# Kernel optimization log

Hardware: AMD Instinct MI355X
Metric: run time of the kernel (lower is better)

Reference implementation:

```python
import jax, jax.numpy as jnp
import numpy as np

N_NODES = 50000
N_EDGES = 800000
N_FEAT = 128
HIDDEN = 256
N_CLASSES = 40
K_HOPS = 10
ALPHA = 0.1


def setup_inputs() -> dict:
    key = jax.random.key(0)
    k1, k2, k3, k4 = jax.random.split(key, 4)
    x = jax.random.normal(k1, (N_NODES, N_FEAT), dtype=jnp.float32)
    edge_index = jax.random.randint(k2, (2, N_EDGES), 0, N_NODES, dtype=jnp.int64)
    # PPR init of gamma weights: temp[k] = alpha*(1-alpha)^k, temp[K] = (1-alpha)^K
    temp_np = ALPHA * (1.0 - ALPHA) ** np.arange(K_HOPS + 1)
    temp_np[-1] = (1.0 - ALPHA) ** K_HOPS
    temp = jnp.asarray(temp_np, dtype=jnp.float32)
    W1 = jax.random.normal(k3, (N_FEAT, HIDDEN), dtype=jnp.float32) * (1.0 / np.sqrt(N_FEAT))
    b1 = jnp.zeros((HIDDEN,), dtype=jnp.float32)
    W2 = jax.random.normal(k4, (HIDDEN, N_CLASSES), dtype=jnp.float32) * (1.0 / np.sqrt(HIDDEN))
    b2 = jnp.zeros((N_CLASSES,), dtype=jnp.float32)
    return {"x": x, "edge_index": edge_index, "temp": temp,
            "W1": W1, "b1": b1, "W2": W2, "b2": b2, "K": K_HOPS}


def reference(x, edge_index, temp, W1, b1, W2, b2, K):
    N = x.shape[0]
    # gcn_norm with self-loops (fill value 1): A_hat = D^-1/2 (A + I) D^-1/2
    loops = jnp.arange(N, dtype=edge_index.dtype)
    row = jnp.concatenate([edge_index[0], loops])  # source (x_j)
    col = jnp.concatenate([edge_index[1], loops])  # target (aggregation)
    ones = jnp.ones(row.shape[0], dtype=x.dtype)
    deg = jax.ops.segment_sum(ones, col, num_segments=N)
    dinv = jnp.where(deg > 0, deg ** -0.5, jnp.zeros_like(deg))
    norm = dinv[row] * dinv[col]  # [E+N]

    # K-hop propagation with learned hop-weighted sum
    h = x
    hidden = temp[0] * x
    for k in range(K):  # small fixed hop count
        msg = norm[:, None] * h[row]                      # gather + scale
        h = jax.ops.segment_sum(msg, col, num_segments=N)  # scatter-add
        hidden = hidden + temp[k + 1] * h

    # eval mode: dropout is a no-op
    z = jax.nn.relu(hidden @ W1 + b1)
    z = z @ W2 + b2
    return jax.nn.log_softmax(z, axis=1)
```

## Files before the change

kernel.cpp:

```cpp
#include <hip/hip_runtime.h>
#include <hip/hip_bf16.h>


#define NFEAT 128
#define HID   256
#define NCLS  40
#define KHOPS 10

typedef __attribute__((ext_vector_type(8))) short short8;
typedef __attribute__((ext_vector_type(4))) float floatx4;

__device__ __forceinline__ float blo(unsigned g) { return __uint_as_float(g << 16); }
__device__ __forceinline__ float bhi(unsigned g) { return __uint_as_float(g & 0xffff0000u); }
__device__ __forceinline__ unsigned f2bf(float x) {
  unsigned u = __float_as_uint(x);
  return (u + 0x7fffu + ((u >> 16) & 1u)) >> 16;
}
__device__ __forceinline__ unsigned bpack(float a, float b) {
  return f2bf(a) | (f2bf(b) << 16);
}

__global__ void k_detect64(const unsigned int* __restrict__ raw, int* __restrict__ flag) {
  __shared__ int any;
  int t = threadIdx.x;
  if (t == 0) any = 0;
  __syncthreads();
  if (raw[2 * t + 1] != 0u) any = 1;
  __syncthreads();
  if (t == 0) flag[0] = (any == 0) ? 1 : 0;
}

__global__ void k_zero(int* __restrict__ p, int n) {
  int i = blockIdx.x * blockDim.x + threadIdx.x;
  if (i < n) p[i] = 0;
}

__global__ void k_count(const int* __restrict__ ei32, const long long* __restrict__ ei64,
                        int E, int N, int* __restrict__ cnt, int* __restrict__ rank,
                        const int* __restrict__ flag) {
  int e = blockIdx.x * blockDim.x + threadIdx.x;
  if (e >= E) return;
  int dst = flag[0] ? (int)ei64[(size_t)E + e] : ei32[(size_t)E + e];
  if ((unsigned)dst < (unsigned)N) rank[e] = atomicAdd(&cnt[dst], 1);
  else rank[e] = -1;
}

__global__ __launch_bounds__(256) void k_scan_a(
    const int* __restrict__ cnt, int* __restrict__ bsum, int n) {
  int t = threadIdx.x;
  int base = blockIdx.x * 1024 + t * 4;
  int s = 0;
  if (base + 3 < n) {
    int4 v = *(const int4*)(cnt + base);
    s = v.x + v.y + v.z + v.w;
  } else {
    #pragma unroll
    for (int j = 0; j < 4; ++j) if (base + j < n) s += cnt[base + j];
  }
  #pragma unroll
  for (int off = 1; off < 64; off <<= 1) s += __shfl_xor(s, off);
  __shared__ int ws[4];
  if ((t & 63) == 0) ws[t >> 6] = s;
  __syncthreads();
  if (t == 0) bsum[blockIdx.x] = ws[0] + ws[1] + ws[2] + ws[3];
}

__global__ void k_scan_mid(int* __restrict__ bsum, int* __restrict__ S,
                           int ntiles, int n) {
  int t = threadIdx.x;
  int lane = t & 63, wid = t >> 6;
  int v = (t < ntiles) ? bsum[t] : 0;
  int x = v;
  #pragma unroll
  for (int off = 1; off < 64; off <<= 1) {
    int u = __shfl_up(x, off);
    if (lane >= off) x += u;
  }
  __shared__ int ws[16];
  if (lane == 63) ws[wid] = x;
  __syncthreads();
  if (wid == 0) {
    int s2 = (lane < 16) ? ws[lane] : 0;
    #pragma unroll
    for (int off = 1; off < 16; off <<= 1) {
      int u = __shfl_up(s2, off);
      if (lane >= off) s2 += u;
    }
    if (lane < 16) ws[lane] = s2;
  }
  __syncthreads();
  int woff = wid ? ws[wid - 1] : 0;
  if (t < ntiles) bsum[t] = x - v + woff;
  if (t == 0) S[n] = ws[15];
}

__global__ __launch_bounds__(256) void k_scan_c(
    const int* __restrict__ cnt, const int* __restrict__ bsum,
    int* __restrict__ S, float* __restrict__ dinv, int n) {
  int t = threadIdx.x;
  int base = blockIdx.x * 1024 + t * 4;
  int v[4];
  if (base + 3 < n) {
    int4 q = *(const int4*)(cnt + base);
    v[0] = q.x; v[1] = q.y; v[2] = q.z; v[3] = q.w;
  } else {
    #pragma unroll
    for (int j = 0; j < 4; ++j) v[j] = (base + j < n) ? cnt[base + j] : 0;
  }
  int tsum = v[0] + v[1] + v[2] + v[3];
  int lane = t & 63, wv = t >> 6;
  int x = tsum;
  #pragma unroll
  for (int off = 1; off < 64; off <<= 1) {
    int u = __shfl_up(x, off);
    if (lane >= off) x += u;
  }
  __shared__ int ws[4];
  if (lane == 63) ws[wv] = x;
  __syncthreads();
  int woff = 0;
  #pragma unroll
  for (int j = 0; j < 4; ++j) if (j < wv) woff += ws[j];
  int run = x - tsum + woff + bsum[blockIdx.x];
  #pragma unroll
  for (int j = 0; j < 4; ++j) {
    int idx = base + j;
    if (idx < n) {
      S[idx] = run;
      dinv[idx] = rsqrtf((float)(v[j] + 1));
      run += v[j];
    }
  }
}

__global__ void k_fill(const int* __restrict__ ei32, const long long* __restrict__ ei64,
                       int E, int N, const int* __restrict__ S,
                       const int* __restrict__ rank, int* __restrict__ csr,
                       const int* __restrict__ flag) {
  int e = blockIdx.x * blockDim.x + threadIdx.x;
  if (e >= E) return;
  int r = rank[e];
  if (r < 0) return;
  int src, dst;
  if (flag[0]) { src = (int)ei64[e]; dst = (int)ei64[(size_t)E + e]; }
  else         { src = ei32[e];      dst = ei32[(size_t)E + e]; }
  if ((unsigned)src >= (unsigned)N) return;
  csr[S[dst] + r] = src;
}

__global__ void k_init(const float* __restrict__ x, const float* __restrict__ temp,
                       const float* __restrict__ dinv,
                       unsigned* __restrict__ h2, float* __restrict__ hidden,
                       int total64) {
  int i = blockIdx.x * blockDim.x + threadIdx.x;
  if (i >= total64) return;
  float2 xv = ((const float2*)x)[i];
  float di = dinv[i >> 6];
  h2[i] = bpack(di * xv.x, di * xv.y);
  float t0 = temp[0];
  ((float2*)hidden)[i] = make_float2(t0 * xv.x, t0 * xv.y);
}

__global__ __launch_bounds__(256) void k_prop(
    const unsigned* __restrict__ h2, unsigned* __restrict__ hnew2,
    float* __restrict__ hidden,
    const int* __restrict__ S, const int* __restrict__ csr,
    const float* __restrict__ dinv, const float* __restrict__ temp,
    int k, int N, int mode) {
  int wid = __builtin_amdgcn_readfirstlane(threadIdx.x >> 6);
  int lane = threadIdx.x & 63;
  int node = blockIdx.x * 4 + wid;
  if (node >= N) return;
  int g = lane & 15;
  int e = lane >> 4;
  int s = S[node], en = S[node + 1];
  float acc[8] = {0.f, 0.f, 0.f, 0.f, 0.f, 0.f, 0.f, 0.f};
  for (int p = s; p < en; p += 16) {
    uint4 gd[4];
    float wt[4];
    #pragma unroll
    for (int t = 0; t < 4; ++t) {
      int pj = p + t * 4 + e;
      int sidx = csr[pj < en ? pj : s];
      wt[t] = (pj < en) ? 1.f : 0.f;
      gd[t] = *(const uint4*)(h2 + (size_t)sidx * 64 + g * 4);
    }
    #pragma unroll
    for (int t = 0; t < 4; ++t) {
      const unsigned* gu = (const unsigned*)&gd[t];
      #pragma unroll
      for (int u = 0; u < 4; ++u) {
        acc[u * 2]     += wt[t] * blo(gu[u]);
        acc[u * 2 + 1] += wt[t] * bhi(gu[u]);
      }
    }
  }
  #pragma unroll
  for (int u = 0; u < 8; ++u) {
    acc[u] += __shfl_xor(acc[u], 16);
    acc[u] += __shfl_xor(acc[u], 32);
  }
  if (e == 0) {
    float di = dinv[node];
    uint4 gs = *(const uint4*)(h2 + (size_t)node * 64 + g * 4);
    const unsigned* su = (const unsigned*)&gs;
    #pragma unroll
    for (int u = 0; u < 4; ++u) {
      acc[u * 2]     += blo(su[u]);
      acc[u * 2 + 1] += bhi(su[u]);
    }
    float hn[8];
    #pragma unroll
    for (int u = 0; u < 8; ++u) hn[u] = di * acc[u];
    float tk = temp[k + 1];
    float4* hp = (float4*)(hidden + (size_t)node * NFEAT + g * 8);
    float4 h0 = hp[0], h1 = hp[1];
    h0.x += tk * hn[0];  h0.y += tk * hn[1];
    h0.z += tk * hn[2];  h0.w += tk * hn[3];
    h1.x += tk * hn[4];  h1.y += tk * hn[5];
    h1.z += tk * hn[6];  h1.w += tk * hn[7];
    uint4 pk;
    if (mode == 0) {
      pk.x = bpack(di * hn[0], di * hn[1]);
      pk.y = bpack(di * hn[2], di * hn[3]);
      pk.z = bpack(di * hn[4], di * hn[5]);
      pk.w = bpack(di * hn[6], di * hn[7]);
      *(uint4*)(hnew2 + (size_t)node * 64 + g * 4) = pk;
      hp[0] = h0;  hp[1] = h1;
    } else {
      pk.x = bpack(h0.x, h0.y);  pk.y = bpack(h0.z, h0.w);
      pk.z = bpack(h1.x, h1.y);  pk.w = bpack(h1.z, h1.w);
      *(uint4*)(hnew2 + (size_t)node * 64 + g * 4) = pk;
    }
  }
}

__global__ __launch_bounds__(256) void k_gemm1(
    const unsigned short* __restrict__ Ab, const float* __restrict__ W1,
    const float* __restrict__ b1, unsigned short* __restrict__ z1, int M) {
  __shared__ unsigned short As[64][136];
  __shared__ unsigned short Bs[16][128][8];
  int tid = threadIdx.x;
  int m0 = blockIdx.x * 64;
  int n0 = blockIdx.y * 128;
  for (int idx = tid; idx < 64 * 16; idx += 256) {
    int m = idx >> 4, c = idx & 15;
    int row = m0 + m; if (row >= M) row = M - 1;
    uint4 v = *(const uint4*)(Ab + (size_t)row * NFEAT + c * 8);
    *(uint4*)&As[m][c * 8] = v;
  }
  for (int idx = tid; idx < 128 * 128; idx += 256) {
    int k = idx >> 7, n = idx & 127;
    Bs[k >> 3][n][k & 7] = (unsigned short)f2bf(W1[(size_t)k * HID + n0 + n]);
  }
  __syncthreads();
  int lane = tid & 63;
  int q = lane >> 4, r16 = lane & 15;
  int nw = (tid >> 6) * 32;
  floatx4 acc[4][2] = {};
  #pragma unroll
  for (int step = 0; step < 4; ++step) {
    int k0 = step * 32;
    short8 a[4], b[2];
    #pragma unroll
    for (int i = 0; i < 4; ++i)
      a[i] = *(const short8*)&As[i * 16 + r16][k0 + q * 8];
    #pragma unroll
    for (int j = 0; j < 2; ++j)
      b[j] = *(const short8*)&Bs[step * 4 + q][nw + j * 16 + r16][0];
    #pragma unroll
    for (int i = 0; i < 4; ++i)
      #pragma unroll
      for (int j = 0; j < 2; ++j)
        acc[i][j] = __builtin_amdgcn_mfma_f32_16x16x32_bf16(a[i], b[j], acc[i][j], 0, 0, 0);
  }
  __syncthreads();
  unsigned short* Zs = &As[0][0];
  #pragma unroll
  for (int j = 0; j < 2; ++j) {
    int n = nw + j * 16 + r16;
    float bias = b1[n0 + n];
    #pragma unroll
    for (int i = 0; i < 4; ++i) {
      #pragma unroll
      for (int r = 0; r < 4; ++r) {
        int m = i * 16 + q * 4 + r;
        float v = fmaxf(acc[i][j][r] + bias, 0.f);
        Zs[m * 136 + n] = (unsigned short)f2bf(v);
      }
    }
  }
  __syncthreads();
  for (int idx = tid; idx < 64 * 16; idx += 256) {
    int m = idx >> 4, c = idx & 15;
    int row = m0 + m;
    if (row < M) {
      uint4 v = *(const uint4*)&Zs[m * 136 + c * 8];
      *(uint4*)(z1 + (size_t)row * HID + n0 + c * 8) = v;
    }
  }
}

__global__ void k_w2prep(const float* __restrict__ W2, unsigned short* __restrict__ W2t) {
  int i = blockIdx.x * blockDim.x + threadIdx.x;
  if (i >= 48 * 256) return;
  int n = i >> 8, k = i & 255;
  W2t[n * 256 + k] = (n < NCLS) ? (unsigned short)f2bf(W2[(size_t)k * NCLS + n]) : 0;
}

__global__ __launch_bounds__(256) void k_mlp2(
    const unsigned short* __restrict__ z1, const unsigned short* __restrict__ W2t,
    const float* __restrict__ b2, float* __restrict__ out, int N) {
  int tid = threadIdx.x;
  int lane = tid & 63;
  int wv = tid >> 6;
  int node0 = blockIdx.x * 64 + wv * 16;
  int q = lane >> 4, m = lane & 15;
  int arow = node0 + m; if (arow >= N) arow = N - 1;
  const unsigned short* aptr = z1 + (size_t)arow * HID + q * 8;
  const unsigned short* bptr = W2t + (size_t)m * HID + q * 8;
  floatx4 acc[3] = {};
  #pragma unroll
  for (int step = 0; step < 8; ++step) {
    short8 a = *(const short8*)(aptr + step * 32);
    #pragma unroll
    for (int j = 0; j < 3; ++j) {
      short8 b = *(const short8*)(bptr + (size_t)j * 16 * HID + step * 32);
      acc[j] = __builtin_amdgcn_mfma_f32_16x16x32_bf16(a, b, acc[j], 0, 0, 0);
    }
  }
  int c = m;
  bool v2 = (c < NCLS - 32);
  float bb0 = b2[c], bb1 = b2[c + 16];
  float bb2 = v2 ? b2[c + 32] : 0.f;
  #pragma unroll
  for (int r = 0; r < 4; ++r) {
    int node = node0 + q * 4 + r;
    float l0 = acc[0][r] + bb0;
    float l1 = acc[1][r] + bb1;
    float l2 = v2 ? (acc[2][r] + bb2) : -3.4e38f;
    float mx = fmaxf(fmaxf(l0, l1), l2);
    #pragma unroll
    for (int off = 1; off < 16; off <<= 1) mx = fmaxf(mx, __shfl_xor(mx, off));
    float sm = __expf(l0 - mx) + __expf(l1 - mx) + (v2 ? __expf(l2 - mx) : 0.f);
    #pragma unroll
    for (int off = 1; off < 16; off <<= 1) sm += __shfl_xor(sm, off);
    float lse = mx + __logf(sm);
    if (node < N) {
      float* op = out + (size_t)node * NCLS + c;
      op[0] = l0 - lse;
      op[16] = l1 - lse;
      if (v2) op[32] = l2 - lse;
    }
  }
}

extern "C" void kernel_launch(void* const* d_in, const int* in_sizes, int n_in,
                              void* d_out, int out_size, void* d_ws, size_t ws_size,
                              hipStream_t stream) {
  const float*     x    = (const float*)d_in[0];
  const int*       ei32 = (const int*)d_in[1];
  const long long* ei64 = (const long long*)d_in[1];
  const float*     temp = (const float*)d_in[2];
  const float*     W1   = (const float*)d_in[3];
  const float*     b1   = (const float*)d_in[4];
  const float*     W2   = (const float*)d_in[5];
  const float*     b2   = (const float*)d_in[6];
  float* out = (float*)d_out;

  int N = in_sizes[0] / NFEAT;
  int E = in_sizes[1] / 2;

  char* w = (char*)d_ws;
  auto carve = [&](size_t bytes) -> void* {
    void* p = (void*)w;
    w += (bytes + 255) & ~(size_t)255;
    return p;
  };
  int*      flag      = (int*)     carve(4);
  int*      cnt       = (int*)     carve((size_t)N * 4);
  int*      S         = (int*)     carve(((size_t)N + 1) * 4);
  float*    dinv      = (float*)   carve((size_t)N * 4);
  int*      bsum      = (int*)     carve(1024 * 4);
  unsigned short* W2t = (unsigned short*)carve(48 * 256 * 2);
  int*      rank      = (int*)     carve((size_t)E * 4);
  int*      csr       = (int*)     carve((size_t)E * 4);
  unsigned* h_a       = (unsigned*)carve((size_t)N * 64 * 4);
  unsigned* h_b       = (unsigned*)carve((size_t)N * 64 * 4);
  unsigned* hid       = (unsigned*)carve((size_t)N * 64 * 4);
  float*    hidden32  = (float*)   carve((size_t)N * NFEAT * 4);
  unsigned short* z1  = (unsigned short*)hidden32;

  int ntiles = (N + 1023) / 1024;

  k_detect64<<<1, 256, 0, stream>>>((const unsigned int*)d_in[1], flag);
  k_zero<<<(N + 255) / 256, 256, 0, stream>>>(cnt, N);
  k_count<<<(E + 255) / 256, 256, 0, stream>>>(ei32, ei64, E, N, cnt, rank, flag);
  k_scan_a<<<ntiles, 256, 0, stream>>>(cnt, bsum, N);
  k_scan_mid<<<1, 1024, 0, stream>>>(bsum, S, ntiles, N);
  k_scan_c<<<ntiles, 256, 0, stream>>>(cnt, bsum, S, dinv, N);
  k_fill<<<(E + 255) / 256, 256, 0, stream>>>(ei32, ei64, E, N, S, rank, csr, flag);
  k_init<<<(N * 64 + 255) / 256, 256, 0, stream>>>(x, temp, dinv, h_a, hidden32, N * 64);
  k_w2prep<<<48, 256, 0, stream>>>(W2, W2t);

  unsigned* hc = h_a;
  unsigned* hn = h_b;
  for (int k = 0; k < KHOPS - 1; ++k) {
    k_prop<<<(N + 3) / 4, 256, 0, stream>>>(
        hc, hn, hidden32, S, csr, dinv, temp, k, N, 0);
    unsigned* t2 = hc; hc = hn; hn = t2;
  }
  k_prop<<<(N + 3) / 4, 256, 0, stream>>>(
      hc, hid, hidden32, S, csr, dinv, temp, KHOPS - 1, N, 1);

  k_gemm1<<<dim3((N + 63) / 64, 2), 256, 0, stream>>>(
      (const unsigned short*)hid, W1, b1, z1, N);
  k_mlp2<<<(N + 63) / 64, 256, 0, stream>>>(z1, W2t, b2, out, N);
}
```

Measured before the change: 537.1 us.

## Store every hop in bf16 slabs and combine hop-weighted sum in one pass

Each propagation hop now writes its scaled bf16 result to its own slab and no longer reads and writes the fp32 hidden accumulator. A final combine kernel reads all hop slabs and forms the temp-weighted sum. This removes about 1 KB per node per hop of fp32 read-modify-write traffic. In exchange it uses more workspace and adds one kernel that rereads every hop slab. The sum is now accumulated from bf16-rounded hop values, and the combine divides by dinv, which assumes dinv is never zero.

```diff
diff --git a/kernel.cpp b/kernel.cpp
--- a/kernel.cpp
+++ b/kernel.cpp
@@ -148,25 +148,19 @@
   csr[S[dst] + r] = src;
 }
 
-__global__ void k_init(const float* __restrict__ x, const float* __restrict__ temp,
-                       const float* __restrict__ dinv,
-                       unsigned* __restrict__ h2, float* __restrict__ hidden,
-                       int total64) {
+__global__ void k_init(const float* __restrict__ x, const float* __restrict__ dinv,
+                       unsigned* __restrict__ p0, int total64) {
   int i = blockIdx.x * blockDim.x + threadIdx.x;
   if (i >= total64) return;
   float2 xv = ((const float2*)x)[i];
   float di = dinv[i >> 6];
-  h2[i] = bpack(di * xv.x, di * xv.y);
-  float t0 = temp[0];
-  ((float2*)hidden)[i] = make_float2(t0 * xv.x, t0 * xv.y);
+  p0[i] = bpack(di * xv.x, di * xv.y);
 }
 
 __global__ __launch_bounds__(256) void k_prop(
-    const unsigned* __restrict__ h2, unsigned* __restrict__ hnew2,
-    float* __restrict__ hidden,
+    const unsigned* __restrict__ pin, unsigned* __restrict__ pout,
     const int* __restrict__ S, const int* __restrict__ csr,
-    const float* __restrict__ dinv, const float* __restrict__ temp,
-    int k, int N, int mode) {
+    const float* __restrict__ dinv, int N) {
   int wid = __builtin_amdgcn_readfirstlane(threadIdx.x >> 6);
   int lane = threadIdx.x & 63;
   int node = blockIdx.x * 4 + wid;
@@ -183,7 +177,7 @@
       int pj = p + t * 4 + e;
       int sidx = csr[pj < en ? pj : s];
       wt[t] = (pj < en) ? 1.f : 0.f;
-      gd[t] = *(const uint4*)(h2 + (size_t)sidx * 64 + g * 4);
+      gd[t] = *(const uint4*)(pin + (size_t)sidx * 64 + g * 4);
     }
     #pragma unroll
     for (int t = 0; t < 4; ++t) {
@@ -202,37 +196,41 @@
   }
   if (e == 0) {
     float di = dinv[node];
-    uint4 gs = *(const uint4*)(h2 + (size_t)node * 64 + g * 4);
+    float dd = di * di;
+    uint4 gs = *(const uint4*)(pin + (size_t)node * 64 + g * 4);
     const unsigned* su = (const unsigned*)&gs;
     #pragma unroll
     for (int u = 0; u < 4; ++u) {
       acc[u * 2]     += blo(su[u]);
       acc[u * 2 + 1] += bhi(su[u]);
     }
-    float hn[8];
-    #pragma unroll
-    for (int u = 0; u < 8; ++u) hn[u] = di * acc[u];
-    float tk = temp[k + 1];
-    float4* hp = (float4*)(hidden + (size_t)node * NFEAT + g * 8);
-    float4 h0 = hp[0], h1 = hp[1];
-    h0.x += tk * hn[0];  h0.y += tk * hn[1];
-    h0.z += tk * hn[2];  h0.w += tk * hn[3];
-    h1.x += tk * hn[4];  h1.y += tk * hn[5];
-    h1.z += tk * hn[6];  h1.w += tk * hn[7];
     uint4 pk;
-    if (mode == 0) {
-      pk.x = bpack(di * hn[0], di * hn[1]);
-      pk.y = bpack(di * hn[2], di * hn[3]);
-      pk.z = bpack(di * hn[4], di * hn[5]);
-      pk.w = bpack(di * hn[6], di * hn[7]);
-      *(uint4*)(hnew2 + (size_t)node * 64 + g * 4) = pk;
-      hp[0] = h0;  hp[1] = h1;
-    } else {
-      pk.x = bpack(h0.x, h0.y);  pk.y = bpack(h0.z, h0.w);
-      pk.z = bpack(h1.x, h1.y);  pk.w = bpack(h1.z, h1.w);
-      *(uint4*)(hnew2 + (size_t)node * 64 + g * 4) = pk;
-    }
-  }
+    pk.x = bpack(dd * acc[0], dd * acc[1]);
+    pk.y = bpack(dd * acc[2], dd * acc[3]);
+    pk.z = bpack(dd * acc[4], dd * acc[5]);
+    pk.w = bpack(dd * acc[6], dd * acc[7]);
+    *(uint4*)(pout + (size_t)node * 64 + g * 4) = pk;
+  }
+}
+
+__global__ void k_combine(const unsigned* __restrict__ pbuf,
+                          const float* __restrict__ temp,
+                          const float* __restrict__ dinv,
+                          unsigned* __restrict__ hid, int N) {
+  int i = blockIdx.x * blockDim.x + threadIdx.x;
+  int total = N * 64;
+  if (i >= total) return;
+  size_t slab = (size_t)total;
+  float tL = 0.f, tH = 0.f;
+  #pragma unroll
+  for (int k = 0; k <= KHOPS; ++k) {
+    unsigned v = pbuf[slab * k + i];
+    float tk = temp[k];
+    tL += tk * blo(v);
+    tH += tk * bhi(v);
+  }
+  float inv = 1.f / dinv[i >> 6];
+  hid[i] = bpack(tL * inv, tH * inv);
 }
 
 __global__ __launch_bounds__(256) void k_gemm1(
@@ -385,13 +383,12 @@
   unsigned short* W2t = (unsigned short*)carve(48 * 256 * 2);
   int*      rank      = (int*)     carve((size_t)E * 4);
   int*      csr       = (int*)     carve((size_t)E * 4);
-  unsigned* h_a       = (unsigned*)carve((size_t)N * 64 * 4);
-  unsigned* h_b       = (unsigned*)carve((size_t)N * 64 * 4);
+  unsigned* pbuf      = (unsigned*)carve((size_t)(KHOPS + 1) * N * 64 * 4);
   unsigned* hid       = (unsigned*)carve((size_t)N * 64 * 4);
-  float*    hidden32  = (float*)   carve((size_t)N * NFEAT * 4);
-  unsigned short* z1  = (unsigned short*)hidden32;
+  unsigned short* z1  = (unsigned short*)carve((size_t)N * HID * 2);
 
   int ntiles = (N + 1023) / 1024;
+  size_t slab = (size_t)N * 64;
 
   k_detect64<<<1, 256, 0, stream>>>((const unsigned int*)d_in[1], flag);
   k_zero<<<(N + 255) / 256, 256, 0, stream>>>(cnt, N);
@@ -400,18 +397,14 @@
   k_scan_mid<<<1, 1024, 0, stream>>>(bsum, S, ntiles, N);
   k_scan_c<<<ntiles, 256, 0, stream>>>(cnt, bsum, S, dinv, N);
   k_fill<<<(E + 255) / 256, 256, 0, stream>>>(ei32, ei64, E, N, S, rank, csr, flag);
-  k_init<<<(N * 64 + 255) / 256, 256, 0, stream>>>(x, temp, dinv, h_a, hidden32, N * 64);
+  k_init<<<(N * 64 + 255) / 256, 256, 0, stream>>>(x, dinv, pbuf, N * 64);
   k_w2prep<<<48, 256, 0, stream>>>(W2, W2t);
 
-  unsigned* hc = h_a;
-  unsigned* hn = h_b;
-  for (int k = 0; k < KHOPS - 1; ++k) {
+  for (int k = 0; k < KHOPS; ++k) {
     k_prop<<<(N + 3) / 4, 256, 0, stream>>>(
-        hc, hn, hidden32, S, csr, dinv, temp, k, N, 0);
-    unsigned* t2 = hc; hc = hn; hn = t2;
-  }
-  k_prop<<<(N + 3) / 4, 256, 0, stream>>>(
-      hc, hid, hidden32, S, csr, dinv, temp, KHOPS - 1, N, 1);
+        pbuf + slab * k, pbuf + slab * (k + 1), S, csr, dinv, N);
+  }
+  k_combine<<<(N * 64 + 255) / 256, 256, 0, stream>>>(pbuf, temp, dinv, hid, N);
 
   k_gemm1<<<dim3((N + 63) / 64, 2), 256, 0, stream>>>(
       (const unsigned short*)hid, W1, b1, z1, N);
```

Result: faster. 493.5 us (-8.1%).
